# Optimization experiments

Hardware: AMD Instinct MI355X
Metric: run time of the kernel (lower is better)

The kernel has to match this reference:

```python
import jax, jax.numpy as jnp
import numpy as np

COMMITMENT_COST = 0.25


def setup_inputs() -> dict:
    key = jax.random.key(0)
    k1, k2 = jax.random.split(key)
    B, C, L, H, W = 4, 64, 16, 32, 32
    K = 1024
    inputs = jax.random.normal(k1, (B, C, L, H, W), dtype=jnp.float32)
    # matches torch init: uniform_(-1/K, 1/K)
    codebook = jax.random.uniform(k2, (K, C), dtype=jnp.float32,
                                  minval=-1.0 / K, maxval=1.0 / K)
    return {"inputs": inputs, "codebook": codebook}


def reference(inputs, codebook):
    B, C, L, H, W = inputs.shape
    # [B,C,L,H,W] -> [N, D] with D == embedding_dim == C
    x = jnp.transpose(inputs, (0, 2, 3, 4, 1)).reshape(-1, C).astype(jnp.float32)
    cb = codebook.astype(jnp.float32)
    # squared euclidean distances (argmin identical to p=2 cdist argmin)
    d2 = (jnp.sum(x * x, axis=1, keepdims=True)
          - 2.0 * (x @ cb.T)
          + jnp.sum(cb * cb, axis=1))  # [N, K]
    encoding_indices = jnp.argmin(d2, axis=1)  # [N]
    # one-hot @ codebook == direct gather
    quantized = cb[encoding_indices].astype(inputs.dtype)  # [N, D]
    quantized = jnp.transpose(quantized.reshape(B, L, H, W, C), (0, 4, 1, 2, 3))
    e_latent_loss = jnp.mean((jax.lax.stop_gradient(quantized) - inputs) ** 2)
    q_latent_loss = jnp.mean((quantized - jax.lax.stop_gradient(inputs)) ** 2)
    loss = q_latent_loss + COMMITMENT_COST * e_latent_loss
    # straight-through estimator
    quantized_st = inputs + jax.lax.stop_gradient(quantized - inputs)
    return quantized_st, loss, encoding_indices[:, None]
```

## Files before the change

kernel.cpp:

```cpp
#include <hip/hip_runtime.h>

constexpr int Cc   = 64;
constexpr int Kc   = 1024;
constexpr int Dc   = 64;
constexpr int LHWc = 16 * 32 * 32;
constexpr int Nc   = 4 * LHWc;
constexpr int QSIZE    = 4 * Cc * LHWc;
constexpr int OFF_LOSS = QSIZE;
constexpr int OFF_IDX  = QSIZE + 1;

constexpr int BLK_ROWS = 256;
constexpr int MBW      = 32;
constexpr int XPAD     = 68;

typedef __attribute__((ext_vector_type(8))) short short8;
typedef __attribute__((ext_vector_type(4))) float f32x4;

static __device__ __forceinline__ unsigned short f2bf(float f) {
    unsigned u = __float_as_uint(f);
    u += 0x7FFFu + ((u >> 16) & 1u);
    return (unsigned short)(u >> 16);
}
static __device__ __forceinline__ float bf2f(unsigned short h) {
    return __uint_as_float(((unsigned)h) << 16);
}

__global__ void vq_prep(const float* __restrict__ cb, float* __restrict__ out,
                        unsigned short* __restrict__ cbh,
                        unsigned short* __restrict__ cbl,
                        float* __restrict__ c2)
{
    const int k = blockIdx.x * 256 + threadIdx.x;
    if (k == 0) out[OFF_LOSS] = 0.0f;
    if (k >= Kc) return;
    const float* c = cb + (size_t)k * Dc;
    float s = 0.f;
#pragma unroll
    for (int d = 0; d < Dc; ++d) {
        float v = c[d];
        s = __builtin_fmaf(v, v, s);
        unsigned short h = f2bf(v);
        cbh[(size_t)k * Dc + d] = h;
        cbl[(size_t)k * Dc + d] = f2bf(v - bf2f(h));
    }
    c2[k] = s;
}

__global__ __launch_bounds__(512, 2) void vq_main(
    const float* __restrict__ in, const float* __restrict__ codebook,
    const unsigned short* __restrict__ cbh,
    const unsigned short* __restrict__ cbl,
    const float* __restrict__ c2g, float* __restrict__ out)
{
    __shared__ float xs[BLK_ROWS][XPAD];
    __shared__ float xs2[BLK_ROWS];
    __shared__ int   cand[BLK_ROWS];

    const int tid  = threadIdx.x;
    const int lane = tid & 63;
    const int w    = __builtin_amdgcn_readfirstlane(tid >> 6);
    const int col  = lane & 15;
    const int g    = lane >> 4;

    const int bq = blockIdx.x >> 6;
    const int p0 = (blockIdx.x & 63) * BLK_ROWS;
    const size_t inBase = (size_t)bq * (Cc * LHWc) + p0;

#pragma unroll
    for (int i = 0; i < 32; ++i) {
        int idx = i * 512 + tid;
        int d = idx >> 8, row = idx & 255;
        xs[row][d] = in[inBase + (size_t)d * LHWc + row];
    }
    __syncthreads();

    if (tid < BLK_ROWS) {
        float s = 0.f;
#pragma unroll
        for (int d = 0; d < Dc; ++d) s = __builtin_fmaf(xs[tid][d], xs[tid][d], s);
        xs2[tid] = s;
    }
    __syncthreads();

    const int wrow0 = w * MBW;

    short8 xh[2][2], xl[2][2];
#pragma unroll
    for (int t = 0; t < 2; ++t) {
#pragma unroll
        for (int kt = 0; kt < 2; ++kt) {
            const float* px = &xs[wrow0 + t * 16 + col][kt * 32 + g * 8];
            f32x4 v0 = *(const f32x4*)px;
            f32x4 v1 = *(const f32x4*)(px + 4);
            short8 h8, l8;
#pragma unroll
            for (int j = 0; j < 4; ++j) {
                unsigned short ha = f2bf(v0[j]);
                h8[j]     = (short)ha;
                l8[j]     = (short)f2bf(v0[j] - bf2f(ha));
                unsigned short hb = f2bf(v1[j]);
                h8[4 + j] = (short)hb;
                l8[4 + j] = (short)f2bf(v1[j] - bf2f(hb));
            }
            xh[t][kt] = h8; xl[t][kt] = l8;
        }
    }

    float x2r[2][4];
#pragma unroll
    for (int t = 0; t < 2; ++t)
#pragma unroll
        for (int r = 0; r < 4; ++r)
            x2r[t][r] = xs2[wrow0 + t * 16 + g * 4 + r];

    float bV[2][4], sV[2][4];
    int   bK[2][4], sK[2][4];
#pragma unroll
    for (int t = 0; t < 2; ++t)
#pragma unroll
        for (int r = 0; r < 4; ++r) {
            bV[t][r] = 3.4e38f; sV[t][r] = 3.4e38f; bK[t][r] = 0; sK[t][r] = 0;
        }

    const unsigned short* bhp = cbh + (size_t)col * Dc + g * 8;
    const unsigned short* blp = cbl + (size_t)col * Dc + g * 8;

    short8 bh0 = *(const short8*)(bhp);
    short8 bh1 = *(const short8*)(bhp + 32);
    short8 bl0 = *(const short8*)(blp);
    short8 bl1 = *(const short8*)(blp + 32);

#pragma unroll 1
    for (int ct = 0; ct < 64; ++ct) {
        short8 ch0 = bh0, ch1 = bh1, cl0 = bl0, cl1 = bl1;
        bhp += 16 * Dc; blp += 16 * Dc;
        if (ct < 63) {
            bh0 = *(const short8*)(bhp);
            bh1 = *(const short8*)(bhp + 32);
            bl0 = *(const short8*)(blp);
            bl1 = *(const short8*)(blp + 32);
        }

        f32x4 acc0 = {0.f, 0.f, 0.f, 0.f};
        f32x4 acc1 = {0.f, 0.f, 0.f, 0.f};
        acc0 = __builtin_amdgcn_mfma_f32_16x16x32_bf16(xh[0][0], ch0, acc0, 0, 0, 0);
        acc0 = __builtin_amdgcn_mfma_f32_16x16x32_bf16(xh[0][1], ch1, acc0, 0, 0, 0);
        acc0 = __builtin_amdgcn_mfma_f32_16x16x32_bf16(xh[0][0], cl0, acc0, 0, 0, 0);
        acc0 = __builtin_amdgcn_mfma_f32_16x16x32_bf16(xh[0][1], cl1, acc0, 0, 0, 0);
        acc0 = __builtin_amdgcn_mfma_f32_16x16x32_bf16(xl[0][0], ch0, acc0, 0, 0, 0);
        acc0 = __builtin_amdgcn_mfma_f32_16x16x32_bf16(xl[0][1], ch1, acc0, 0, 0, 0);

        acc1 = __builtin_amdgcn_mfma_f32_16x16x32_bf16(xh[1][0], ch0, acc1, 0, 0, 0);
        acc1 = __builtin_amdgcn_mfma_f32_16x16x32_bf16(xh[1][1], ch1, acc1, 0, 0, 0);
        acc1 = __builtin_amdgcn_mfma_f32_16x16x32_bf16(xh[1][0], cl0, acc1, 0, 0, 0);
        acc1 = __builtin_amdgcn_mfma_f32_16x16x32_bf16(xh[1][1], cl1, acc1, 0, 0, 0);
        acc1 = __builtin_amdgcn_mfma_f32_16x16x32_bf16(xl[1][0], ch0, acc1, 0, 0, 0);
        acc1 = __builtin_amdgcn_mfma_f32_16x16x32_bf16(xl[1][1], ch1, acc1, 0, 0, 0);

        const int   kcol = ct * 16 + col;
        const float c2v  = c2g[kcol];
#pragma unroll
        for (int t = 0; t < 2; ++t) {
#pragma unroll
            for (int r = 0; r < 4; ++r) {
                float a  = (t == 0) ? acc0[r] : acc1[r];
                float d2 = __builtin_fmaf(-2.f, a, x2r[t][r]) + c2v;
                bool  c1 = d2 < bV[t][r];
                float mx  = c1 ? bV[t][r] : d2;
                int   mxk = c1 ? bK[t][r] : kcol;
                bV[t][r] = c1 ? d2 : bV[t][r];
                bK[t][r] = c1 ? kcol : bK[t][r];
                bool  cc2 = mx < sV[t][r];
                sV[t][r] = cc2 ? mx : sV[t][r];
                sK[t][r] = cc2 ? mxk : sK[t][r];
            }
        }
    }

#pragma unroll
    for (int m = 1; m < 16; m <<= 1) {
#pragma unroll
        for (int t = 0; t < 2; ++t) {
#pragma unroll
            for (int r = 0; r < 4; ++r) {
                float ob  = __shfl_xor(bV[t][r], m, 64);
                int   obk = __shfl_xor(bK[t][r], m, 64);
                float os  = __shfl_xor(sV[t][r], m, 64);
                int   osk = __shfl_xor(sK[t][r], m, 64);
                bool  c1 = ob < bV[t][r];
                float nb  = c1 ? ob : bV[t][r];
                int   nbk = c1 ? obk : bK[t][r];
                float mx  = c1 ? bV[t][r] : ob;
                int   mxk = c1 ? bK[t][r] : obk;
                bool  c3 = os < sV[t][r];
                float ms  = c3 ? os : sV[t][r];
                int   msk = c3 ? osk : sK[t][r];
                bool  c4 = mx < ms;
                sV[t][r] = c4 ? mx : ms;
                sK[t][r] = c4 ? mxk : msk;
                bV[t][r] = nb; bK[t][r] = nbk;
            }
        }
    }
    if (col == 0) {
#pragma unroll
        for (int t = 0; t < 2; ++t)
#pragma unroll
            for (int r = 0; r < 4; ++r)
                cand[wrow0 + t * 16 + g * 4 + r] = bK[t][r] | (sK[t][r] << 16);
    }
    __syncthreads();

    int kw = 0;
    if (lane < 32) {
        const int row = wrow0 + lane;
        const int cd  = cand[row];
        const int bk  = cd & 0xFFFF;
        const int sk  = cd >> 16;
        const float* cb0 = codebook + (size_t)bk * Dc;
        const float* cb1 = codebook + (size_t)sk * Dc;
        float a0 = 0.f, a1 = 0.f;
#pragma unroll 8
        for (int d = 0; d < Dc; ++d) {
            float xv = xs[row][d];
            a0 = __builtin_fmaf(xv, cb0[d], a0);
            a1 = __builtin_fmaf(xv, cb1[d], a1);
        }
        const float x2v = xs2[row];
        float db  = __builtin_fmaf(-2.f, a0, x2v) + c2g[bk];
        float dsv = __builtin_fmaf(-2.f, a1, x2v) + c2g[sk];
        kw = bk;
        if (dsv < db || (dsv == db && sk < bk)) kw = sk;
        out[OFF_IDX + blockIdx.x * BLK_ROWS + row] = (float)kw;
    }

    const int rowh = lane & 31;
    const int chh  = lane >> 5;
    const int kwv  = __shfl(kw, rowh, 64);
    const int row  = wrow0 + rowh;
    const float* cbw = codebook + (size_t)kwv * Dc + chh * 32;
    float* qout = out + inBase + row;
    float ls = 0.f;
#pragma unroll
    for (int cc = 0; cc < 32; ++cc) {
        int c = chh * 32 + cc;
        float q = cbw[cc];
        qout[(size_t)c * LHWc] = q;
        float e = q - xs[row][c];
        ls = __builtin_fmaf(e, e, ls);
    }
#pragma unroll
    for (int off = 32; off > 0; off >>= 1) ls += __shfl_down(ls, off, 64);
    if (lane == 0) atomicAdd(&out[OFF_LOSS], ls * (1.25f / (float)QSIZE));
}

extern "C" void kernel_launch(void* const* d_in, const int* in_sizes, int n_in,
                              void* d_out, int out_size, void* d_ws, size_t ws_size,
                              hipStream_t stream) {
    const float* in = (const float*)d_in[0];
    const float* cb = (const float*)d_in[1];
    float* out = (float*)d_out;
    (void)in_sizes; (void)n_in; (void)out_size; (void)ws_size;

    unsigned short* cbh = (unsigned short*)d_ws;
    unsigned short* cbl = cbh + (size_t)Kc * Dc;
    float*          c2  = (float*)(cbl + (size_t)Kc * Dc);

    vq_prep<<<dim3(Kc / 256), dim3(256), 0, stream>>>(cb, out, cbh, cbl, c2);
    vq_main<<<dim3(Nc / BLK_ROWS), dim3(512), 0, stream>>>(in, cb, cbh, cbl, c2, out);
}
```

Before: 169.7 us.

## Split codebook across waves with smaller row blocks and parallel candidate rescoring

Shrinks each block to 64 rows and splits the 1024-entry codebook into four quarters, one per wave group, so every wave scans 256 codes instead of all 1024. The grid grows to 1024 blocks and the occupancy hint rises. Codebook norms are cached in shared memory with a +0.25 bias, which keeps the biased distance positive for the packed-key comparison, and x2 is dropped from the inner loop. The final rescoring of 8 candidates per row is spread over 8 threads using vectorized loads and a packed 64-bit shuffle min, and the quantized write is spread over all 512 threads. The trade-offs are more atomics on the loss, more per-block setup, and reading the codebook from global memory once per block.

```diff
diff --git a/kernel.cpp b/kernel.cpp
--- a/kernel.cpp
+++ b/kernel.cpp
@@ -9,8 +9,7 @@
 constexpr int OFF_LOSS = QSIZE;
 constexpr int OFF_IDX  = QSIZE + 1;
 
-constexpr int BLK_ROWS = 256;
-constexpr int MBW      = 32;
+constexpr int BLK_ROWS = 64;
 constexpr int XPAD     = 68;
 
 typedef __attribute__((ext_vector_type(8))) short short8;
@@ -46,30 +45,39 @@
     c2[k] = s;
 }
 
-__global__ __launch_bounds__(512, 2) void vq_main(
+__global__ __launch_bounds__(512, 4) void vq_main(
     const float* __restrict__ in, const float* __restrict__ codebook,
     const unsigned short* __restrict__ cbh,
     const unsigned short* __restrict__ cbl,
     const float* __restrict__ c2g, float* __restrict__ out)
 {
-    __shared__ float xs[BLK_ROWS][XPAD];
-    __shared__ float xs2[BLK_ROWS];
-    __shared__ int   cand[BLK_ROWS];
+    __shared__ float    xs[BLK_ROWS][XPAD];
+    __shared__ float    xs2[BLK_ROWS];
+    __shared__ float    c2bs[Kc];
+    __shared__ unsigned cand[BLK_ROWS][4];
+    __shared__ int      kws[BLK_ROWS];
 
     const int tid  = threadIdx.x;
     const int lane = tid & 63;
     const int w    = __builtin_amdgcn_readfirstlane(tid >> 6);
     const int col  = lane & 15;
     const int g    = lane >> 4;
-
-    const int bq = blockIdx.x >> 6;
-    const int p0 = (blockIdx.x & 63) * BLK_ROWS;
+    const int rg   = w >> 2;
+    const int qq   = w & 3;
+    const int wrow0 = rg * 32;
+    const int kbase = qq * 256;
+
+    const int bq = blockIdx.x >> 8;
+    const int p0 = (blockIdx.x & 255) * BLK_ROWS;
     const size_t inBase = (size_t)bq * (Cc * LHWc) + p0;
 
-#pragma unroll
-    for (int i = 0; i < 32; ++i) {
+    c2bs[tid]       = c2g[tid] + 0.25f;
+    c2bs[tid + 512] = c2g[tid + 512] + 0.25f;
+
+#pragma unroll
+    for (int i = 0; i < 8; ++i) {
         int idx = i * 512 + tid;
-        int d = idx >> 8, row = idx & 255;
+        int d = idx >> 6, row = idx & 63;
         xs[row][d] = in[inBase + (size_t)d * LHWc + row];
     }
     __syncthreads();
@@ -80,9 +88,6 @@
         for (int d = 0; d < Dc; ++d) s = __builtin_fmaf(xs[tid][d], xs[tid][d], s);
         xs2[tid] = s;
     }
-    __syncthreads();
-
-    const int wrow0 = w * MBW;
 
     short8 xh[2][2], xl[2][2];
 #pragma unroll
@@ -106,13 +111,6 @@
         }
     }
 
-    float x2r[2][4];
-#pragma unroll
-    for (int t = 0; t < 2; ++t)
-#pragma unroll
-        for (int r = 0; r < 4; ++r)
-            x2r[t][r] = xs2[wrow0 + t * 16 + g * 4 + r];
-
     float bV[2][4], sV[2][4];
     int   bK[2][4], sK[2][4];
 #pragma unroll
@@ -122,19 +120,22 @@
             bV[t][r] = 3.4e38f; sV[t][r] = 3.4e38f; bK[t][r] = 0; sK[t][r] = 0;
         }
 
-    const unsigned short* bhp = cbh + (size_t)col * Dc + g * 8;
-    const unsigned short* blp = cbl + (size_t)col * Dc + g * 8;
+    const unsigned short* bhp = cbh + (size_t)(kbase + col) * Dc + g * 8;
+    const unsigned short* blp = cbl + (size_t)(kbase + col) * Dc + g * 8;
 
     short8 bh0 = *(const short8*)(bhp);
     short8 bh1 = *(const short8*)(bhp + 32);
     short8 bl0 = *(const short8*)(blp);
     short8 bl1 = *(const short8*)(blp + 32);
 
+    int kcolv = kbase + col;
+
 #pragma unroll 1
-    for (int ct = 0; ct < 64; ++ct) {
+    for (int ct = 0; ct < 16; ++ct) {
+        const float c2bv = c2bs[kcolv];
         short8 ch0 = bh0, ch1 = bh1, cl0 = bl0, cl1 = bl1;
         bhp += 16 * Dc; blp += 16 * Dc;
-        if (ct < 63) {
+        if (ct < 15) {
             bh0 = *(const short8*)(bhp);
             bh1 = *(const short8*)(bhp + 32);
             bl0 = *(const short8*)(blp);
@@ -144,37 +145,36 @@
         f32x4 acc0 = {0.f, 0.f, 0.f, 0.f};
         f32x4 acc1 = {0.f, 0.f, 0.f, 0.f};
         acc0 = __builtin_amdgcn_mfma_f32_16x16x32_bf16(xh[0][0], ch0, acc0, 0, 0, 0);
+        acc1 = __builtin_amdgcn_mfma_f32_16x16x32_bf16(xh[1][0], ch0, acc1, 0, 0, 0);
         acc0 = __builtin_amdgcn_mfma_f32_16x16x32_bf16(xh[0][1], ch1, acc0, 0, 0, 0);
+        acc1 = __builtin_amdgcn_mfma_f32_16x16x32_bf16(xh[1][1], ch1, acc1, 0, 0, 0);
         acc0 = __builtin_amdgcn_mfma_f32_16x16x32_bf16(xh[0][0], cl0, acc0, 0, 0, 0);
+        acc1 = __builtin_amdgcn_mfma_f32_16x16x32_bf16(xh[1][0], cl0, acc1, 0, 0, 0);
         acc0 = __builtin_amdgcn_mfma_f32_16x16x32_bf16(xh[0][1], cl1, acc0, 0, 0, 0);
+        acc1 = __builtin_amdgcn_mfma_f32_16x16x32_bf16(xh[1][1], cl1, acc1, 0, 0, 0);
         acc0 = __builtin_amdgcn_mfma_f32_16x16x32_bf16(xl[0][0], ch0, acc0, 0, 0, 0);
+        acc1 = __builtin_amdgcn_mfma_f32_16x16x32_bf16(xl[1][0], ch0, acc1, 0, 0, 0);
         acc0 = __builtin_amdgcn_mfma_f32_16x16x32_bf16(xl[0][1], ch1, acc0, 0, 0, 0);
-
-        acc1 = __builtin_amdgcn_mfma_f32_16x16x32_bf16(xh[1][0], ch0, acc1, 0, 0, 0);
-        acc1 = __builtin_amdgcn_mfma_f32_16x16x32_bf16(xh[1][1], ch1, acc1, 0, 0, 0);
-        acc1 = __builtin_amdgcn_mfma_f32_16x16x32_bf16(xh[1][0], cl0, acc1, 0, 0, 0);
-        acc1 = __builtin_amdgcn_mfma_f32_16x16x32_bf16(xh[1][1], cl1, acc1, 0, 0, 0);
-        acc1 = __builtin_amdgcn_mfma_f32_16x16x32_bf16(xl[1][0], ch0, acc1, 0, 0, 0);
         acc1 = __builtin_amdgcn_mfma_f32_16x16x32_bf16(xl[1][1], ch1, acc1, 0, 0, 0);
 
-        const int   kcol = ct * 16 + col;
-        const float c2v  = c2g[kcol];
 #pragma unroll
         for (int t = 0; t < 2; ++t) {
 #pragma unroll
             for (int r = 0; r < 4; ++r) {
                 float a  = (t == 0) ? acc0[r] : acc1[r];
-                float d2 = __builtin_fmaf(-2.f, a, x2r[t][r]) + c2v;
-                bool  c1 = d2 < bV[t][r];
-                float mx  = c1 ? bV[t][r] : d2;
-                int   mxk = c1 ? bK[t][r] : kcol;
-                bV[t][r] = c1 ? d2 : bV[t][r];
-                bK[t][r] = c1 ? kcol : bK[t][r];
-                bool  cc2 = mx < sV[t][r];
-                sV[t][r] = cc2 ? mx : sV[t][r];
-                sK[t][r] = cc2 ? mxk : sK[t][r];
+                float v  = __builtin_fmaf(-2.f, a, c2bv);
+                bool  c1 = v < bV[t][r];
+                float nb  = c1 ? v : bV[t][r];
+                int   nbk = c1 ? kcolv : bK[t][r];
+                float mx  = c1 ? bV[t][r] : v;
+                int   mxk = c1 ? bK[t][r] : kcolv;
+                bool  c2_ = mx < sV[t][r];
+                sV[t][r] = c2_ ? mx : sV[t][r];
+                sK[t][r] = c2_ ? mxk : sK[t][r];
+                bV[t][r] = nb; bK[t][r] = nbk;
             }
         }
+        kcolv += 16;
     }
 
 #pragma unroll
@@ -207,51 +207,62 @@
         for (int t = 0; t < 2; ++t)
 #pragma unroll
             for (int r = 0; r < 4; ++r)
-                cand[wrow0 + t * 16 + g * 4 + r] = bK[t][r] | (sK[t][r] << 16);
+                cand[wrow0 + t * 16 + g * 4 + r][qq] =
+                    (unsigned)bK[t][r] | ((unsigned)sK[t][r] << 16);
     }
     __syncthreads();
 
-    int kw = 0;
-    if (lane < 32) {
-        const int row = wrow0 + lane;
-        const int cd  = cand[row];
-        const int bk  = cd & 0xFFFF;
-        const int sk  = cd >> 16;
-        const float* cb0 = codebook + (size_t)bk * Dc;
-        const float* cb1 = codebook + (size_t)sk * Dc;
-        float a0 = 0.f, a1 = 0.f;
-#pragma unroll 8
-        for (int d = 0; d < Dc; ++d) {
-            float xv = xs[row][d];
-            a0 = __builtin_fmaf(xv, cb0[d], a0);
-            a1 = __builtin_fmaf(xv, cb1[d], a1);
-        }
-        const float x2v = xs2[row];
-        float db  = __builtin_fmaf(-2.f, a0, x2v) + c2g[bk];
-        float dsv = __builtin_fmaf(-2.f, a1, x2v) + c2g[sk];
-        kw = bk;
-        if (dsv < db || (dsv == db && sk < bk)) kw = sk;
-        out[OFF_IDX + blockIdx.x * BLK_ROWS + row] = (float)kw;
-    }
-
-    const int rowh = lane & 31;
-    const int chh  = lane >> 5;
-    const int kwv  = __shfl(kw, rowh, 64);
-    const int row  = wrow0 + rowh;
-    const float* cbw = codebook + (size_t)kwv * Dc + chh * 32;
-    float* qout = out + inBase + row;
-    float ls = 0.f;
-#pragma unroll
-    for (int cc = 0; cc < 32; ++cc) {
-        int c = chh * 32 + cc;
-        float q = cbw[cc];
-        qout[(size_t)c * LHWc] = q;
-        float e = q - xs[row][c];
-        ls = __builtin_fmaf(e, e, ls);
-    }
-#pragma unroll
-    for (int off = 32; off > 0; off >>= 1) ls += __shfl_down(ls, off, 64);
-    if (lane == 0) atomicAdd(&out[OFF_LOSS], ls * (1.25f / (float)QSIZE));
+    {
+        const int row = tid >> 3;
+        const int ci  = tid & 7;
+        const unsigned cd = cand[row][ci >> 1];
+        const int k = (ci & 1) ? (int)(cd >> 16) : (int)(cd & 0xFFFFu);
+        const float* cbr = codebook + (size_t)k * Dc;
+        float a = 0.f;
+#pragma unroll
+        for (int d4 = 0; d4 < 16; ++d4) {
+            f32x4 cv = *(const f32x4*)(cbr + d4 * 4);
+            const float* xr = &xs[row][d4 * 4];
+            a = __builtin_fmaf(xr[0], cv[0], a);
+            a = __builtin_fmaf(xr[1], cv[1], a);
+            a = __builtin_fmaf(xr[2], cv[2], a);
+            a = __builtin_fmaf(xr[3], cv[3], a);
+        }
+        float d2 = __builtin_fmaf(-2.f, a, xs2[row]) + c2g[k];
+        unsigned long long pk =
+            ((unsigned long long)__float_as_uint(d2) << 32) | (unsigned)k;
+#pragma unroll
+        for (int m = 1; m < 8; m <<= 1) {
+            unsigned long long o = __shfl_xor(pk, m, 64);
+            pk = o < pk ? o : pk;
+        }
+        if (ci == 0) {
+            const int kwin = (int)(pk & 0xFFFFFFFFu);
+            kws[row] = kwin;
+            out[OFF_IDX + (size_t)blockIdx.x * BLK_ROWS + row] = (float)kwin;
+        }
+    }
+    __syncthreads();
+
+    {
+        const int row = tid & 63;
+        const int cp  = tid >> 6;
+        const int kw  = kws[row];
+        const float* cbw = codebook + (size_t)kw * Dc + cp * 8;
+        float* qout = out + inBase + row;
+        float ls = 0.f;
+#pragma unroll
+        for (int j = 0; j < 8; ++j) {
+            const int c = cp * 8 + j;
+            float qv = cbw[j];
+            qout[(size_t)c * LHWc] = qv;
+            float e = qv - xs[row][c];
+            ls = __builtin_fmaf(e, e, ls);
+        }
+#pragma unroll
+        for (int off = 32; off > 0; off >>= 1) ls += __shfl_down(ls, off, 64);
+        if (lane == 0) atomicAdd(&out[OFF_LOSS], ls * (1.25f / (float)QSIZE));
+    }
 }
 
 extern "C" void kernel_launch(void* const* d_in, const int* in_sizes, int n_in,
```

New measurement: 213.3 us. +25.7%, slower.
